# Performance work log

Hardware: AMD Instinct MI355X
Metric: run time of the kernel (lower is better)

## Reference

```python
import jax, jax.numpy as jnp
import numpy as np

NUM_EXPERTS_TOTAL = 9  # 8 routed + 1 shared (shared expert is also routed via softmax in this module)
TOP_K = 2


def setup_inputs() -> dict:
    key = jax.random.key(0)
    k0, k1, k2, k3, k4 = jax.random.split(key, 5)
    B, S, H, I = 2, 2048, 1024, 2816
    E = NUM_EXPERTS_TOTAL
    x = jax.random.normal(k0, (B, S, H), dtype=jnp.float32)
    Wr = (jax.random.normal(k1, (H, E), dtype=jnp.float32) * 0.02)          # router (no bias)
    Wg = (jax.random.normal(k2, (E, H, I), dtype=jnp.float32) * 0.02)       # gate_proj per expert
    Wu = (jax.random.normal(k3, (E, H, I), dtype=jnp.float32) * 0.02)       # up_proj per expert
    Wd = (jax.random.normal(k4, (E, I, H), dtype=jnp.float32) * 0.02)       # down_proj per expert
    return {"x": x, "Wr": Wr, "Wg": Wg, "Wu": Wu, "Wd": Wd}


def reference(x, Wr, Wg, Wu, Wd):
    B, S, H = x.shape
    E = NUM_EXPERTS_TOTAL
    T = B * S

    # Router: softmax over all 9 experts, then top-2 and renormalize
    logits = jnp.einsum('bsh,he->bse', x, Wr)
    probs = jax.nn.softmax(logits, axis=-1)
    topk_w, topk_idx = jax.lax.top_k(probs, TOP_K)                 # [B,S,K]
    topk_w = topk_w / jnp.sum(topk_w, axis=-1, keepdims=True)

    xf = x.reshape(T, H)
    wf = topk_w.reshape(T, TOP_K)
    idxf = topk_idx.reshape(T, TOP_K)

    # Per-token combine weight for each expert (0 if not selected)
    cw = jnp.zeros((T, E), dtype=x.dtype).at[jnp.arange(T)[:, None], idxf].add(wf)  # [T,E]

    # SwiGLU MLP for every expert (tokens with cw==0 contribute nothing)
    gate = jax.nn.silu(jnp.einsum('th,ehi->tei', xf, Wg))          # [T,E,I]
    hidden = gate * jnp.einsum('th,ehi->tei', xf, Wu)              # [T,E,I]
    out = jnp.einsum('tei,eih,te->th', hidden, Wd, cw)             # weighted combine
    return out.reshape(B, S, H)
```

## Files before the change

kernel.cpp:

```cpp
#include <hip/hip_runtime.h>
#include <cstdint>
#include <cstddef>

#define T_TOK 4096
#define H_DIM 1024
#define I_DIM 2816
#define E_NUM 9
#define MAXTILE 76

typedef __bf16 bf16;
typedef bf16 bf16x4 __attribute__((ext_vector_type(4)));
typedef bf16 bf16x8 __attribute__((ext_vector_type(8)));
typedef float f32x4 __attribute__((ext_vector_type(4)));

constexpr int BM = 128, BN = 128, BK = 32;

#define GL16(gp, lp)                                                                   \
  __builtin_amdgcn_global_load_lds((const __attribute__((address_space(1))) void*)(gp), \
                                   (__attribute__((address_space(3))) void*)(lp), 16, 0, 0)

__global__ __launch_bounds__(256) void k_xcast(const float* __restrict__ x, bf16* __restrict__ xb) {
  size_t i = ((size_t)blockIdx.x * 256 + threadIdx.x) * 8;
  float4 a = *reinterpret_cast<const float4*>(x + i);
  float4 b = *reinterpret_cast<const float4*>(x + i + 4);
  bf16x8 v;
  v[0]=(bf16)a.x; v[1]=(bf16)a.y; v[2]=(bf16)a.z; v[3]=(bf16)a.w;
  v[4]=(bf16)b.x; v[5]=(bf16)b.y; v[6]=(bf16)b.z; v[7]=(bf16)b.w;
  *reinterpret_cast<bf16x8*>(xb + i) = v;
}

__global__ __launch_bounds__(256) void k_transpose(const float* __restrict__ in,
                                                   bf16* __restrict__ out, int R, int C) {
  const float* src = in + (size_t)blockIdx.z * R * C;
  bf16* dst = out + (size_t)blockIdx.z * R * C;
  __shared__ bf16 tile[64][72];
  int r0 = blockIdx.y * 64, c0 = blockIdx.x * 64;
  int t = threadIdx.x;
  int tr = t >> 4, tc = (t & 15) * 4;
#pragma unroll
  for (int it = 0; it < 4; ++it) {
    int r = tr + it * 16;
    float4 v = *reinterpret_cast<const float4*>(src + (size_t)(r0 + r) * C + c0 + tc);
    bf16x4 w; w[0]=(bf16)v.x; w[1]=(bf16)v.y; w[2]=(bf16)v.z; w[3]=(bf16)v.w;
    *reinterpret_cast<bf16x4*>(&tile[r][tc]) = w;
  }
  __syncthreads();
#pragma unroll
  for (int it = 0; it < 4; ++it) {
    int oc = tr + it * 16;
    bf16x4 w;
    w[0] = tile[tc + 0][oc]; w[1] = tile[tc + 1][oc];
    w[2] = tile[tc + 2][oc]; w[3] = tile[tc + 3][oc];
    *reinterpret_cast<bf16x4*>(dst + (size_t)(c0 + oc) * R + r0 + tc) = w;
  }
}

__global__ __launch_bounds__(256) void k_router(const float* __restrict__ x,
                                                const float* __restrict__ Wr,
                                                int* __restrict__ ridx,
                                                float* __restrict__ rw,
                                                int* __restrict__ counts) {
  int lane = threadIdx.x & 63;
  int wid  = threadIdx.x >> 6;
  int t = blockIdx.x * 4 + wid;
  const float* xr = x + (size_t)t * H_DIM;
  float acc[E_NUM];
#pragma unroll
  for (int e = 0; e < E_NUM; ++e) acc[e] = 0.f;
  for (int h = lane; h < H_DIM; h += 64) {
    float xv = xr[h];
    const float* wr = Wr + h * E_NUM;
#pragma unroll
    for (int e = 0; e < E_NUM; ++e) acc[e] += xv * wr[e];
  }
#pragma unroll
  for (int off = 32; off > 0; off >>= 1) {
#pragma unroll
    for (int e = 0; e < E_NUM; ++e) acc[e] += __shfl_xor(acc[e], off);
  }
  if (lane == 0) {
    int i0 = 0;
#pragma unroll
    for (int e = 1; e < E_NUM; ++e) if (acc[e] > acc[i0]) i0 = e;
    int i1 = (i0 == 0) ? 1 : 0;
#pragma unroll
    for (int e = 0; e < E_NUM; ++e) if (e != i0 && acc[e] > acc[i1]) i1 = e;
    float r  = expf(acc[i1] - acc[i0]);
    float w0 = 1.f / (1.f + r);
    float w1 = r / (1.f + r);
    ridx[2 * t]     = i0;
    ridx[2 * t + 1] = i1;
    rw[2 * t]     = w0;
    rw[2 * t + 1] = w1;
    atomicAdd(&counts[i0], 1);
    atomicAdd(&counts[i1], 1);
  }
}

__global__ void k_scan(const int* __restrict__ counts, int* __restrict__ offsets,
                       int* __restrict__ cursor, int* __restrict__ tiles,
                       int* __restrict__ n_tiles) {
  if (threadIdx.x == 0) {
    int s = 0, nt = 0;
    for (int e = 0; e < E_NUM; ++e) {
      offsets[e] = s;
      int c = counts[e];
      for (int pt = 0; pt * BM < c && nt < MAXTILE; ++pt) tiles[nt++] = (e << 16) | pt;
      s += c;
    }
    offsets[E_NUM] = s;
    *n_tiles = nt;
  }
  if (threadIdx.x < E_NUM) cursor[threadIdx.x] = 0;
}

__global__ __launch_bounds__(256) void k_scatter(const int* __restrict__ ridx,
                                                 const int* __restrict__ offsets,
                                                 int* __restrict__ cursor,
                                                 int* __restrict__ perm) {
  int t = blockIdx.x * 256 + threadIdx.x;
  if (t >= T_TOK) return;
#pragma unroll
  for (int k = 0; k < 2; ++k) {
    int e = ridx[2 * t + k];
    int pos = atomicAdd(&cursor[e], 1);
    perm[offsets[e] + pos] = 2 * t + k;
  }
}

__global__ __launch_bounds__(256, 2) void k_gateup(const bf16* __restrict__ xb,
                                                   const bf16* __restrict__ WgT,
                                                   const bf16* __restrict__ WuT,
                                                   const int* __restrict__ perm,
                                                   const int* __restrict__ offsets,
                                                   const int* __restrict__ tiles,
                                                   const int* __restrict__ n_tiles,
                                                   bf16* __restrict__ hidden) {
  if ((int)blockIdx.y >= *n_tiles) return;
  int tv = tiles[blockIdx.y];
  int e = tv >> 16, pt = tv & 0xffff;
  int seg0 = offsets[e], cnt = offsets[e + 1] - seg0;
  int n0 = blockIdx.x * BN;

  __shared__ bf16 As[2][BM * BK];
  __shared__ bf16 Bg[2][BN * BK];
  __shared__ bf16 Bu[2][BN * BK];

  int tid = threadIdx.x, lane = tid & 63, wid = tid >> 6;
  int wm = wid >> 1, wn = wid & 1, l15 = lane & 15, l16 = lane >> 4;

  int srow1 = tid >> 2, srow2 = 64 + (tid >> 2);
  int kc = (tid & 3) * 8;
  int p1 = pt * BM + srow1, p2 = pt * BM + srow2;
  const bf16* a1 = xb + (size_t)(perm[seg0 + (p1 < cnt ? p1 : 0)] >> 1) * H_DIM + kc;
  const bf16* a2 = xb + (size_t)(perm[seg0 + (p2 < cnt ? p2 : 0)] >> 1) * H_DIM + kc;
  const bf16* g1 = WgT + ((size_t)e * I_DIM + n0 + srow1) * H_DIM + kc;
  const bf16* g2 = WgT + ((size_t)e * I_DIM + n0 + srow2) * H_DIM + kc;
  const bf16* u1 = WuT + ((size_t)e * I_DIM + n0 + srow1) * H_DIM + kc;
  const bf16* u2 = WuT + ((size_t)e * I_DIM + n0 + srow2) * H_DIM + kc;

  f32x4 accg[4][4], accu[4][4];
#pragma unroll
  for (int m = 0; m < 4; ++m)
#pragma unroll
    for (int n = 0; n < 4; ++n) {
      accg[m][n] = (f32x4){0.f, 0.f, 0.f, 0.f};
      accu[m][n] = (f32x4){0.f, 0.f, 0.f, 0.f};
    }

  auto STAGE = [&](int b, int kt) {
    int k0 = kt * BK;
    GL16(a1 + k0, &As[b][tid * 8]);  GL16(a2 + k0, &As[b][2048 + tid * 8]);
    GL16(g1 + k0, &Bg[b][tid * 8]);  GL16(g2 + k0, &Bg[b][2048 + tid * 8]);
    GL16(u1 + k0, &Bu[b][tid * 8]);  GL16(u2 + k0, &Bu[b][2048 + tid * 8]);
  };
  auto COMPUTE = [&](int b) {
    bf16x8 af[4], bg[4], bu[4];
#pragma unroll
    for (int m = 0; m < 4; ++m)
      af[m] = *reinterpret_cast<const bf16x8*>(&As[b][(wm * 64 + m * 16 + l15) * BK + l16 * 8]);
#pragma unroll
    for (int n = 0; n < 4; ++n) {
      bg[n] = *reinterpret_cast<const bf16x8*>(&Bg[b][(wn * 64 + n * 16 + l15) * BK + l16 * 8]);
      bu[n] = *reinterpret_cast<const bf16x8*>(&Bu[b][(wn * 64 + n * 16 + l15) * BK + l16 * 8]);
    }
#pragma unroll
    for (int m = 0; m < 4; ++m)
#pragma unroll
      for (int n = 0; n < 4; ++n) {
        accg[m][n] = __builtin_amdgcn_mfma_f32_16x16x32_bf16(af[m], bg[n], accg[m][n], 0, 0, 0);
        accu[m][n] = __builtin_amdgcn_mfma_f32_16x16x32_bf16(af[m], bu[n], accu[m][n], 0, 0, 0);
      }
  };

  constexpr int NT = H_DIM / BK;
  STAGE(0, 0);
  __syncthreads();
  for (int kt = 0; kt < NT; kt += 2) {
    if (kt + 1 < NT) STAGE(1, kt + 1);
    COMPUTE(0);
    __syncthreads();
    if (kt + 2 < NT) STAGE(0, kt + 2);
    COMPUTE(1);
    __syncthreads();
  }

#pragma unroll
  for (int m = 0; m < 4; ++m) {
#pragma unroll
    for (int r = 0; r < 4; ++r) {
      int p_glob = pt * BM + wm * 64 + m * 16 + l16 * 4 + r;
      if (p_glob < cnt) {
        bf16* hrow = hidden + (size_t)(seg0 + p_glob) * I_DIM;
#pragma unroll
        for (int n = 0; n < 4; ++n) {
          int col = n0 + wn * 64 + n * 16 + l15;
          float g = accg[m][n][r];
          float u = accu[m][n][r];
          float h = g / (1.f + __expf(-g)) * u;
          hrow[col] = (bf16)h;
        }
      }
    }
  }
}

__global__ __launch_bounds__(256, 3) void k_down(const bf16* __restrict__ hidden,
                                                 const bf16* __restrict__ WdT,
                                                 const int* __restrict__ perm,
                                                 const int* __restrict__ offsets,
                                                 const int* __restrict__ tiles,
                                                 const int* __restrict__ n_tiles,
                                                 float* __restrict__ pair_out) {
  if ((int)blockIdx.y >= *n_tiles) return;
  int tv = tiles[blockIdx.y];
  int e = tv >> 16, pt = tv & 0xffff;
  int seg0 = offsets[e], cnt = offsets[e + 1] - seg0;
  int n0 = blockIdx.x * BN;

  __shared__ bf16 As[2][BM * BK];
  __shared__ bf16 Bs[2][BN * BK];

  int tid = threadIdx.x, lane = tid & 63, wid = tid >> 6;
  int wm = wid >> 1, wn = wid & 1, l15 = lane & 15, l16 = lane >> 4;

  int srow1 = tid >> 2, srow2 = 64 + (tid >> 2);
  int kc = (tid & 3) * 8;
  int p1 = pt * BM + srow1, p2 = pt * BM + srow2;
  const bf16* a1 = hidden + (size_t)(seg0 + (p1 < cnt ? p1 : 0)) * I_DIM + kc;
  const bf16* a2 = hidden + (size_t)(seg0 + (p2 < cnt ? p2 : 0)) * I_DIM + kc;
  const bf16* b1 = WdT + ((size_t)e * H_DIM + n0 + srow1) * I_DIM + kc;
  const bf16* b2 = WdT + ((size_t)e * H_DIM + n0 + srow2) * I_DIM + kc;

  f32x4 acc[4][4];
#pragma unroll
  for (int m = 0; m < 4; ++m)
#pragma unroll
    for (int n = 0; n < 4; ++n) acc[m][n] = (f32x4){0.f, 0.f, 0.f, 0.f};

  auto STAGE = [&](int b, int kt) {
    int k0 = kt * BK;
    GL16(a1 + k0, &As[b][tid * 8]);  GL16(a2 + k0, &As[b][2048 + tid * 8]);
    GL16(b1 + k0, &Bs[b][tid * 8]);  GL16(b2 + k0, &Bs[b][2048 + tid * 8]);
  };
  auto COMPUTE = [&](int b) {
    bf16x8 af[4], bfr[4];
#pragma unroll
    for (int m = 0; m < 4; ++m)
      af[m] = *reinterpret_cast<const bf16x8*>(&As[b][(wm * 64 + m * 16 + l15) * BK + l16 * 8]);
#pragma unroll
    for (int n = 0; n < 4; ++n)
      bfr[n] = *reinterpret_cast<const bf16x8*>(&Bs[b][(wn * 64 + n * 16 + l15) * BK + l16 * 8]);
#pragma unroll
    for (int m = 0; m < 4; ++m)
#pragma unroll
      for (int n = 0; n < 4; ++n)
        acc[m][n] = __builtin_amdgcn_mfma_f32_16x16x32_bf16(af[m], bfr[n], acc[m][n], 0, 0, 0);
  };

  constexpr int NT = I_DIM / BK;
  STAGE(0, 0);
  __syncthreads();
  for (int kt = 0; kt < NT; kt += 2) {
    if (kt + 1 < NT) STAGE(1, kt + 1);
    COMPUTE(0);
    __syncthreads();
    if (kt + 2 < NT) STAGE(0, kt + 2);
    COMPUTE(1);
    __syncthreads();
  }

#pragma unroll
  for (int m = 0; m < 4; ++m) {
#pragma unroll
    for (int r = 0; r < 4; ++r) {
      int p_glob = pt * BM + wm * 64 + m * 16 + l16 * 4 + r;
      if (p_glob < cnt) {
        int pair = perm[seg0 + p_glob];
        float* orow = pair_out + (size_t)pair * H_DIM;
#pragma unroll
        for (int n = 0; n < 4; ++n) {
          int col = n0 + wn * 64 + n * 16 + l15;
          orow[col] = acc[m][n][r];
        }
      }
    }
  }
}

__global__ __launch_bounds__(256) void k_combine(const float* __restrict__ pair_out,
                                                 const float* __restrict__ rw,
                                                 float* __restrict__ out) {
  int t = blockIdx.x;
  int c = threadIdx.x;
  float w0 = rw[2 * t];
  float w1 = rw[2 * t + 1];
  float4 a = *reinterpret_cast<const float4*>(pair_out + ((size_t)(2 * t)) * H_DIM + c * 4);
  float4 b = *reinterpret_cast<const float4*>(pair_out + ((size_t)(2 * t + 1)) * H_DIM + c * 4);
  float4 o;
  o.x = w0 * a.x + w1 * b.x;
  o.y = w0 * a.y + w1 * b.y;
  o.z = w0 * a.z + w1 * b.z;
  o.w = w0 * a.w + w1 * b.w;
  *reinterpret_cast<float4*>(out + (size_t)t * H_DIM + c * 4) = o;
}

extern "C" void kernel_launch(void* const* d_in, const int* in_sizes, int n_in,
                              void* d_out, int out_size, void* d_ws, size_t ws_size,
                              hipStream_t stream) {
  const float* x  = (const float*)d_in[0];
  const float* Wr = (const float*)d_in[1];
  const float* Wg = (const float*)d_in[2];
  const float* Wu = (const float*)d_in[3];
  const float* Wd = (const float*)d_in[4];
  float* out = (float*)d_out;

  char* ws = (char*)d_ws;
  int*   counts  = (int*)(ws);
  int*   cursor  = (int*)(ws + 256);
  int*   offsets = (int*)(ws + 512);
  int*   n_tiles = (int*)(ws + 768);
  int*   tiles   = (int*)(ws + 1024);
  int*   ridx    = (int*)(ws + 64 * 1024);
  float* rw      = (float*)(ws + 128 * 1024);
  int*   perm    = (int*)(ws + 192 * 1024);
  bf16*  xb      = (bf16*)(ws + (1ull << 20));
  bf16*  WgT     = (bf16*)(ws + (16ull << 20));
  bf16*  WuT     = (bf16*)(ws + (66ull << 20));
  bf16*  WdT     = (bf16*)(ws + (116ull << 20));
  bf16*  hidden  = (bf16*)(ws + (166ull << 20));
  float* pair_out = (float*)(ws + (212ull << 20));

  hipMemsetAsync(counts, 0, 64, stream);
  k_xcast<<<dim3(T_TOK * H_DIM / 2048), dim3(256), 0, stream>>>(x, xb);
  k_transpose<<<dim3(I_DIM / 64, H_DIM / 64, E_NUM), dim3(256), 0, stream>>>(Wg, WgT, H_DIM, I_DIM);
  k_transpose<<<dim3(I_DIM / 64, H_DIM / 64, E_NUM), dim3(256), 0, stream>>>(Wu, WuT, H_DIM, I_DIM);
  k_transpose<<<dim3(H_DIM / 64, I_DIM / 64, E_NUM), dim3(256), 0, stream>>>(Wd, WdT, I_DIM, H_DIM);
  k_router<<<dim3(T_TOK / 4), dim3(256), 0, stream>>>(x, Wr, ridx, rw, counts);
  k_scan<<<dim3(1), dim3(64), 0, stream>>>(counts, offsets, cursor, tiles, n_tiles);
  k_scatter<<<dim3((T_TOK + 255) / 256), dim3(256), 0, stream>>>(ridx, offsets, cursor, perm);
  k_gateup<<<dim3(I_DIM / BN, MAXTILE), dim3(256), 0, stream>>>(
      xb, WgT, WuT, perm, offsets, tiles, n_tiles, hidden);
  k_down<<<dim3(H_DIM / BN, MAXTILE), dim3(256), 0, stream>>>(
      hidden, WdT, perm, offsets, tiles, n_tiles, pair_out);
  k_combine<<<dim3(T_TOK), dim3(256), 0, stream>>>(pair_out, rw, out);
}
```

Baseline: 504.6 us.

## Use partial vmcnt waits for two-stage prefetch and raise gateup occupancy

Both grouped GEMM kernels now keep two LDS stages in flight, waiting only until the older stage's global-to-LDS loads finish (partial vmcnt) rather than draining all loads at each barrier. Scheduling barriers pin the s_barrier so the compiler cannot move memory ops across it. Gate/up launch bounds go from 2 to 3 blocks per SM to raise occupancy, which squeezes registers for the 32 accumulator fragments and may cause spills. The hand-counted vmcnt values must match the number of loads per STAGE, or stale LDS data will be read.

After: 586.4 us. 1.16x slower.

```diff
diff --git a/kernel.cpp b/kernel.cpp
--- a/kernel.cpp
+++ b/kernel.cpp
@@ -18,6 +18,13 @@
 #define GL16(gp, lp)                                                                   \
   __builtin_amdgcn_global_load_lds((const __attribute__((address_space(1))) void*)(gp), \
                                    (__attribute__((address_space(3))) void*)(lp), 16, 0, 0)
+
+#define BARRIER_PINNED()                       \
+  do {                                         \
+    __builtin_amdgcn_sched_barrier(0);         \
+    __builtin_amdgcn_s_barrier();              \
+    __builtin_amdgcn_sched_barrier(0);         \
+  } while (0)
 
 __global__ __launch_bounds__(256) void k_xcast(const float* __restrict__ x, bf16* __restrict__ xb) {
   size_t i = ((size_t)blockIdx.x * 256 + threadIdx.x) * 8;
@@ -128,7 +135,7 @@
   }
 }
 
-__global__ __launch_bounds__(256, 2) void k_gateup(const bf16* __restrict__ xb,
+__global__ __launch_bounds__(256, 3) void k_gateup(const bf16* __restrict__ xb,
                                                    const bf16* __restrict__ WgT,
                                                    const bf16* __restrict__ WuT,
                                                    const int* __restrict__ perm,
@@ -195,15 +202,17 @@
 
   constexpr int NT = H_DIM / BK;
   STAGE(0, 0);
-  __syncthreads();
-  for (int kt = 0; kt < NT; kt += 2) {
-    if (kt + 1 < NT) STAGE(1, kt + 1);
-    COMPUTE(0);
-    __syncthreads();
-    if (kt + 2 < NT) STAGE(0, kt + 2);
-    COMPUTE(1);
-    __syncthreads();
-  }
+  STAGE(1, 1);
+  for (int t = 0; t < NT - 1; ++t) {
+    asm volatile("s_waitcnt vmcnt(6)" ::: "memory");
+    BARRIER_PINNED();
+    COMPUTE(t & 1);
+    BARRIER_PINNED();
+    if (t + 2 < NT) STAGE(t & 1, t + 2);
+  }
+  asm volatile("s_waitcnt vmcnt(0)" ::: "memory");
+  BARRIER_PINNED();
+  COMPUTE((NT - 1) & 1);
 
 #pragma unroll
   for (int m = 0; m < 4; ++m) {
@@ -280,15 +289,17 @@
 
   constexpr int NT = I_DIM / BK;
   STAGE(0, 0);
-  __syncthreads();
-  for (int kt = 0; kt < NT; kt += 2) {
-    if (kt + 1 < NT) STAGE(1, kt + 1);
-    COMPUTE(0);
-    __syncthreads();
-    if (kt + 2 < NT) STAGE(0, kt + 2);
-    COMPUTE(1);
-    __syncthreads();
-  }
+  STAGE(1, 1);
+  for (int t = 0; t < NT - 1; ++t) {
+    asm volatile("s_waitcnt vmcnt(4)" ::: "memory");
+    BARRIER_PINNED();
+    COMPUTE(t & 1);
+    BARRIER_PINNED();
+    if (t + 2 < NT) STAGE(t & 1, t + 2);
+  }
+  asm volatile("s_waitcnt vmcnt(0)" ::: "memory");
+  BARRIER_PINNED();
+  COMPUTE((NT - 1) & 1);
 
 #pragma unroll
   for (int m = 0; m < 4; ++m) {
```
